# Kernel optimization log

Measured on AMD Instinct MI355X. Metric: run time of the kernel, lower is better.

## Reference

```python
import jax, jax.numpy as jnp
import numpy as np
import math

NUM_HEADS = 8
HEAD_DIM = 32  # num_units 256 / 8 heads
TIME_DIM = 8
NEG_BIG = -2.0 ** 32 + 1.0


def _ffn(x, W1, b1, W2, b2):
    # two-layer relu MLP: 1 -> time_dim -> time_dim
    h = jax.nn.relu(x @ W1 + b1)
    return jax.nn.relu(h @ W2 + b2)


def _time_gsm_kernel(t, pW1, pb1, pW2, pb2, sW1, sb1, sW2, sb2, bW1, bb1, bW2, bb2):
    # t: [B, L] timestamps -> kernel [B, L, L]
    tt = t[..., None]  # [B, L, 1]
    period = _ffn(tt, pW1, pb1, pW2, pb2)        # [B, L, td]
    qpq = (2.0 * math.pi) * period * tt           # [B, L, td]
    period_diff = qpq[:, :, None, :] - qpq[:, None, :, :]  # [B, Lq, Lk, td]
    cos_enc = jnp.cos(period_diff)
    sigma = _ffn(tt, sW1, sb1, sW2, sb2)          # [B, L, td]
    sq = sigma[:, :, None, :] + 1e-6              # [B, Lq, 1, td] bcast
    sk = sigma[:, None, :, :] + 1e-6              # [B, 1, Lk, td] bcast
    denom = sq ** 2 + sk ** 2
    t_diff = t[:, :, None] - t[:, None, :]        # [B, Lq, Lk]
    exp_enc = jnp.exp(-(t_diff[..., None] ** 2) / denom)
    local_enc = jnp.sqrt(2.0 * sq * sk / denom)
    basis = _ffn(tt, bW1, bb1, bW2, bb2)          # [B, L, td]
    basis_qk = basis[:, :, None, :] * basis[:, None, :, :]
    return jnp.sum(basis_qk * local_enc * exp_enc * cos_enc, axis=-1)  # [B, L, L]


def setup_inputs() -> dict:
    key = jax.random.key(0)
    ks = jax.random.split(key, 20)
    B, L, U = 4, 1024, 256
    td = TIME_DIM
    inp = {
        'query_input': jax.random.normal(ks[0], (B, L, U), dtype=jnp.float32),
        'input_tensor': jax.random.normal(ks[1], (B, L, U), dtype=jnp.float32),
        'input_mask': jnp.ones((B, L), dtype=jnp.int32),
        'time_inputs': jax.random.uniform(ks[2], (B, L), dtype=jnp.float32) * 100.0,
        'att_bias': jnp.zeros((1,), dtype=jnp.int32),
        'Wq': jax.random.normal(ks[3], (U, U), dtype=jnp.float32) * 0.05,
        'Wk': jax.random.normal(ks[4], (U, U), dtype=jnp.float32) * 0.05,
        'Wv': jax.random.normal(ks[5], (U, U), dtype=jnp.float32) * 0.05,
    }
    names = ['p', 's', 'b']
    i = 6
    for n in names:
        inp[n + 'W1'] = jax.random.normal(ks[i], (1, td), dtype=jnp.float32) * 0.5; i += 1
        inp[n + 'b1'] = jnp.zeros((td,), dtype=jnp.float32)
        inp[n + 'W2'] = jax.random.normal(ks[i], (td, td), dtype=jnp.float32) * 0.5; i += 1
        inp[n + 'b2'] = jnp.zeros((td,), dtype=jnp.float32)
    return inp


def reference(query_input, input_tensor, input_mask, time_inputs, att_bias,
              Wq, Wk, Wv,
              pW1, pb1, pW2, pb2, sW1, sb1, sW2, sb2, bW1, bb1, bW2, bb2):
    B, Lq, U = query_input.shape
    Lk = input_tensor.shape[1]
    H, dh = NUM_HEADS, HEAD_DIM

    Q = (query_input @ Wq).reshape(B, Lq, H, dh).transpose(0, 2, 1, 3)  # [B,H,Lq,dh]
    K = (input_tensor @ Wk).reshape(B, Lk, H, dh).transpose(0, 2, 1, 3)
    V = (input_tensor @ Wv).reshape(B, Lk, H, dh).transpose(0, 2, 1, 3)

    scale = 1.0 / math.sqrt(dh)
    scores = jnp.einsum('bhqd,bhkd->bhqk', Q, K) * scale  # [B,H,Lq,Lk]

    tk = _time_gsm_kernel(time_inputs, pW1, pb1, pW2, pb2,
                          sW1, sb1, sW2, sb2, bW1, bb1, bW2, bb2)  # [B,Lq,Lk]
    scores = scores + tk[:, None, :, :] * scale

    # key padding mask: zero-norm keys get -inf-like score
    key_masks = jnp.sign(jnp.sum(jnp.abs(K), axis=-1))  # [B,H,Lk]
    scores = jnp.where(key_masks[:, :, None, :] == 0.0, NEG_BIG, scores)

    # direction == 'forward': allow strictly row > col (strict causal)
    idx = jnp.arange(Lk)
    causal = (idx[:, None] > idx[None, :]).astype(scores.dtype)  # [Lq,Lk]
    scores = scores + (1.0 - causal) * -10000.0

    attn = jax.nn.softmax(scores, axis=-1)

    query_masks = jnp.sign(jnp.sum(jnp.abs(Q), axis=-1))  # [B,H,Lq]
    attn = attn * query_masks[..., None]
    # dropout rate 0.0 -> identity

    out = jnp.einsum('bhqk,bhkd->bhqd', attn, V)
    out = out.transpose(0, 2, 1, 3).reshape(B, Lq, U)
    out = out * input_mask.astype(jnp.float32)[..., None]
    return out
```

## Files before the change

### kernel.cpp

```cpp
#include <hip/hip_runtime.h>
#include <math.h>

#define B_DIM 4
#define L_DIM 1024
#define H_DIM 8
#define D_DIM 32
#define TD 8
#define NTILES_TOT 1056
#define SCALE 0.17677669529663687f
#define TWO_PI_F 6.2831853071795864769f

typedef unsigned short ushort_t;
typedef __attribute__((ext_vector_type(8))) short short8v;
typedef __attribute__((ext_vector_type(4))) float f32x4;

__device__ __forceinline__ int ntiles_of(int qt) { return (qt >> 1) + 1; }
__device__ __forceinline__ int off_of(int qt) {
  int m = qt >> 1;
  return (qt & 1) ? (m + 1) * (m + 1) : m * m + m;
}

__device__ __forceinline__ ushort_t f2bf(float f) {
  unsigned u = __builtin_bit_cast(unsigned, f);
  u += 0x7FFFu + ((u >> 16) & 1u);
  return (ushort_t)(u >> 16);
}
__device__ __forceinline__ float bf2f(ushort_t h) {
  return __builtin_bit_cast(float, ((unsigned)h) << 16);
}
__device__ __forceinline__ short8v pack84(float4 a, float4 b) {
  short8v r;
  r[0] = (short)f2bf(a.x); r[1] = (short)f2bf(a.y);
  r[2] = (short)f2bf(a.z); r[3] = (short)f2bf(a.w);
  r[4] = (short)f2bf(b.x); r[5] = (short)f2bf(b.y);
  r[6] = (short)f2bf(b.z); r[7] = (short)f2bf(b.w);
  return r;
}

__global__ __launch_bounds__(256) void prep_kernel(
    const float* __restrict__ t_in,
    const float* __restrict__ pW1, const float* __restrict__ pb1,
    const float* __restrict__ pW2, const float* __restrict__ pb2,
    const float* __restrict__ sW1, const float* __restrict__ sb1,
    const float* __restrict__ sW2, const float* __restrict__ sb2,
    const float* __restrict__ bW1, const float* __restrict__ bb1,
    const float* __restrict__ bW2, const float* __restrict__ bb2,
    float* __restrict__ ptf, float* __restrict__ sg, float* __restrict__ bs,
    const float* __restrict__ Xq, const float* __restrict__ Xi,
    ushort_t* __restrict__ Xfq, ushort_t* __restrict__ Xfi,
    const float* __restrict__ Wq, const float* __restrict__ Wk,
    const float* __restrict__ Wv, ushort_t* __restrict__ Wf) {
  const int blk = blockIdx.x;
  const int tid = threadIdx.x;
  if (blk < 512) {
    const int lin = blk * 256 + tid;
    const int i = lin >> 5;
    const int slot = lin & 31;
    const int z = slot >> 3, e = slot & 7;
    if (z == 3) return;
    const float* W1 = (z == 0) ? pW1 : (z == 1) ? sW1 : bW1;
    const float* b1 = (z == 0) ? pb1 : (z == 1) ? sb1 : bb1;
    const float* W2 = (z == 0) ? pW2 : (z == 1) ? sW2 : bW2;
    const float* b2 = (z == 0) ? pb2 : (z == 1) ? sb2 : bb2;
    const double t = (double)t_in[i];
    double acc = (double)b2[e];
#pragma unroll
    for (int d = 0; d < 8; ++d) {
      double hv = t * (double)W1[d] + (double)b1[d];
      hv = hv > 0.0 ? hv : 0.0;
      acc += hv * (double)W2[d * 8 + e];
    }
    acc = acc > 0.0 ? acc : 0.0;
    const size_t o = (size_t)i * TD + e;
    if (z == 0) {
      double pt = acc * t;
      ptf[o] = (float)(pt - floor(pt));
    } else if (z == 1) {
      sg[o] = (float)(acc + 1e-6);
    } else {
      bs[o] = (float)acc;
    }
  } else if (blk < 1536) {
    const int xb = blk - 512;
    const float* X = (xb < 512) ? Xq : Xi;
    ushort_t* O = (xb < 512) ? Xfq : Xfi;
    const int lin = (xb & 511) * 256 + tid;
    const int row = lin >> 5, q = lin & 31;
    const float* src = &X[(size_t)row * 256 + q * 8];
    short8v f = pack84(*(const float4*)src, *(const float4*)(src + 4));
    size_t idx = ((size_t)((row >> 4) * 8 + (q >> 2)) * 64 + (q & 3) * 16 + (row & 15)) * 8;
    *(short8v*)&O[idx] = f;
  } else {
    const int wb = blk - 1536;
    const int z = wb >> 5;
    const float* W = (z == 0) ? Wq : (z == 1) ? Wk : Wv;
    const int lin = (wb & 31) * 256 + tid;
    const int kt = lin >> 10, g = (lin >> 8) & 3, n = lin & 255;
    short8v f;
#pragma unroll
    for (int i2 = 0; i2 < 8; ++i2)
      f[i2] = (short)f2bf(W[(size_t)(kt * 32 + g * 8 + i2) * 256 + n]);
    size_t idx = ((size_t)((z * 8 + kt) * 16 + (n >> 4)) * 64 + g * 16 + (n & 15)) * 8;
    *(short8v*)&Wf[idx] = f;
  }
}

__global__ __launch_bounds__(256) void work_kernel(
    const ushort_t* __restrict__ Xfq, const ushort_t* __restrict__ Xfi,
    const ushort_t* __restrict__ Wf,
    ushort_t* __restrict__ Qf, ushort_t* __restrict__ Kf,
    ushort_t* __restrict__ Vf,
    const float* __restrict__ ptf, const float* __restrict__ sg,
    const float* __restrict__ bs, const float* __restrict__ t_in,
    float* __restrict__ tkbuf) {
  __shared__ float ptq[16][TD], ptk[32][9];
  __shared__ float qs[16][TD], qb[16][TD];
  __shared__ float ks[32][9], kb[32][9];
  __shared__ float trow[16], tcol[32];
  const int blk = blockIdx.x;
  const int tid = threadIdx.x;

  if (blk < 384) {
    const int z = blk >> 7;
    const int rem = blk & 127;
    const int m0t = (rem & 31) * 8;
    const int n0 = (rem >> 5) * 64;
    const ushort_t* Xf = (z == 0) ? Xfq : Xfi;
    const int w = tid >> 6, l = tid & 63, lg = l >> 4, lc = l & 15;
    const int wm = w >> 1, wn = w & 1;

    f32x4 acc[4][2];
#pragma unroll
    for (int mi = 0; mi < 4; ++mi)
#pragma unroll
      for (int ni = 0; ni < 2; ++ni) acc[mi][ni] = (f32x4){0.f, 0.f, 0.f, 0.f};

    for (int kt0 = 0; kt0 < 8; ++kt0) {
      short8v a[4], bfr[2];
#pragma unroll
      for (int mi = 0; mi < 4; ++mi)
        a[mi] = *(const short8v*)&Xf[((size_t)(m0t + wm * 4 + mi) * 8 + kt0) * 512 + l * 8];
#pragma unroll
      for (int ni = 0; ni < 2; ++ni)
        bfr[ni] = *(const short8v*)&Wf[((size_t)(z * 8 + kt0) * 16 + (n0 >> 4) + wn * 2 + ni) * 512 + l * 8];
#pragma unroll
      for (int mi = 0; mi < 4; ++mi)
#pragma unroll
        for (int ni = 0; ni < 2; ++ni)
          acc[mi][ni] = __builtin_amdgcn_mfma_f32_16x16x32_bf16(a[mi], bfr[ni], acc[mi][ni], 0, 0, 0);
    }

#pragma unroll
    for (int mi = 0; mi < 4; ++mi) {
#pragma unroll
      for (int ni = 0; ni < 2; ++ni) {
        const int col = n0 + wn * 32 + ni * 16 + lc;
        const int hh = col >> 5, d = col & 31;
#pragma unroll
        for (int r = 0; r < 4; ++r) {
          const int row = (m0t + wm * 4 + mi) * 16 + lg * 4 + r;
          const int bb = row >> 10, lr = row & (L_DIM - 1);
          const ushort_t bv = f2bf(acc[mi][ni][r]);
          if (z == 2) {
            Vf[(((size_t)(bb * H_DIM + hh) * 32 + (lr >> 5)) * 2 + (d >> 4)) * 512 +
               (((lr >> 3) & 3) * 16 + (d & 15)) * 8 + (lr & 7)] = bv;
          } else {
            ushort_t* of16 = (z == 0) ? Qf : Kf;
            of16[((size_t)((bb * H_DIM + hh) * 64 + (lr >> 4))) * 512 +
                 ((d >> 3) * 16 + (lr & 15)) * 8 + (d & 7)] = bv;
          }
        }
      }
    }
  } else {
    const int lin = blk - 384;
    const int b = lin / NTILES_TOT;
    const int t1 = lin - b * NTILES_TOT;
    int m = (int)sqrtf((float)t1 + 1.0f);
    while (m * m + m > t1) --m;
    while ((m + 1) * (m + 1) + (m + 1) <= t1) ++m;
    const int rem = t1 - (m * m + m);
    int qt, kt;
    if (rem <= m) { qt = 2 * m; kt = rem; }
    else          { qt = 2 * m + 1; kt = rem - (m + 1); }

    const int q0 = qt << 4, k0 = kt << 5;
    if (tid < 16 * TD) {
      int i = tid >> 3, d = tid & 7;
      size_t base = (size_t)(b * L_DIM + q0 + i) * TD + d;
      ptq[i][d] = ptf[base]; qs[i][d] = sg[base]; qb[i][d] = bs[base];
    }
    {
      int j = tid >> 3, d = tid & 7;
      size_t base = (size_t)(b * L_DIM + k0 + j) * TD + d;
      ptk[j][d] = ptf[base]; ks[j][d] = sg[base]; kb[j][d] = bs[base];
    }
    if (tid < 16) trow[tid] = t_in[b * L_DIM + q0 + tid];
    if (tid < 32) tcol[tid] = t_in[b * L_DIM + k0 + tid];
    __syncthreads();
    float* dst = &tkbuf[(size_t)(b * NTILES_TOT + off_of(qt) + kt) * 512];
#pragma unroll
    for (int pp = 0; pp < 2; ++pp) {
      int idx = tid + (pp << 8);
      int lr2 = (idx >> 2) & 63;
      int r = idx & 3;
      int i = ((lr2 >> 4) << 2) | r;
      int j = ((idx >> 8) << 4) | (lr2 & 15);
      float td2 = trow[i] - tcol[j];
      td2 *= td2;
      float a = 0.f;
#pragma unroll
      for (int d = 0; d < TD; ++d) {
        float sqd = qs[i][d], skd = ks[j][d];
        float denom = sqd * sqd + skd * skd;
        float inv = __builtin_amdgcn_rcpf(denom);
        float ee = __expf(-td2 * inv);
        float le = __builtin_amdgcn_sqrtf(2.f * sqd * skd * inv);
        float dq = ptq[i][d] - ptk[j][d];
        float ce = __cosf(TWO_PI_F * dq);
        a += qb[i][d] * kb[j][d] * (le * ee * ce);
      }
      dst[idx] = a;
    }
  }
}

__global__ __launch_bounds__(256) void attn_row0_kernel(
    const ushort_t* __restrict__ Qf, const ushort_t* __restrict__ Kf,
    const ushort_t* __restrict__ Vf, const float* __restrict__ tkbuf,
    const int* __restrict__ imask, float* __restrict__ out) {
  __shared__ __align__(16) ushort_t lds_p[4][1024];
  __shared__ float p_s[L_DIM];
  __shared__ float qsh[D_DIM];
  __shared__ float red[8][33];
  __shared__ float rtmp[4];

  const int h = blockIdx.y;
  const int b = blockIdx.z;
  const int tid = threadIdx.x;
  const int fb = (b * H_DIM + h) * 64;
  const int vb = (b * H_DIM + h) * 32;

  if (blockIdx.x == 16) {
    if (tid < D_DIM)
      qsh[tid] = bf2f(Qf[(size_t)fb * 512 + (tid >> 3) * 128 + (tid & 7)]);
    __syncthreads();

    float lmax = -1e30f;
    for (int j = tid; j < L_DIM; j += 256) {
      int i = j & 15;
      float tkv = tkbuf[(size_t)(b * NTILES_TOT + off_of(j >> 4)) * 512 +
                        (((i >> 2) << 6) | (i & 3))];
      const ushort_t* kp = &Kf[(size_t)(fb + (j >> 4)) * 512 + (j & 15) * 8];
      float dot = 0.f;
#pragma unroll
      for (int o = 0; o < 4; ++o) {
        short8v kv = *(const short8v*)&kp[o * 128];
#pragma unroll
        for (int u = 0; u < 8; ++u) dot += qsh[o * 8 + u] * bf2f((ushort_t)kv[u]);
      }
      float sc = (dot + tkv) * SCALE;
      p_s[j] = sc;
      lmax = fmaxf(lmax, sc);
    }
#pragma unroll
    for (int o = 1; o < 64; o <<= 1) lmax = fmaxf(lmax, __shfl_xor(lmax, o));
    if ((tid & 63) == 0) rtmp[tid >> 6] = lmax;
    __syncthreads();
    const float bmax = fmaxf(fmaxf(rtmp[0], rtmp[1]), fmaxf(rtmp[2], rtmp[3]));
    __syncthreads();

    float lsumv = 0.f;
    for (int j = tid; j < L_DIM; j += 256) {
      float pv = __expf(p_s[j] - bmax);
      p_s[j] = pv;
      lsumv += pv;
    }
#pragma unroll
    for (int o = 1; o < 64; o <<= 1) lsumv += __shfl_xor(lsumv, o);
    if ((tid & 63) == 0) rtmp[tid >> 6] = lsumv;
    __syncthreads();
    const float bsum = rtmp[0] + rtmp[1] + rtmp[2] + rtmp[3];

    const int g = tid >> 5, d = tid & 31;
    float a = 0.f;
    for (int j = g * 128; j < g * 128 + 128; ++j) {
      float v = bf2f(Vf[(((size_t)(vb + (j >> 5))) * 2 + (d >> 4)) * 512 +
                        (((j >> 3) & 3) * 16 + (d & 15)) * 8 + (j & 7)]);
      a = fmaf(p_s[j], v, a);
    }
    red[g][d] = a;
    __syncthreads();
    if (tid < D_DIM) {
      float acc = 0.f;
#pragma unroll
      for (int gg = 0; gg < 8; ++gg) acc += red[gg][tid];
      float qabs = 0.f;
#pragma unroll
      for (int dd = 0; dd < D_DIM; ++dd) qabs += fabsf(qsh[dd]);
      const float qmv = qabs > 0.f ? 1.f : 0.f;
      out[((size_t)b * L_DIM) * 256 + h * D_DIM + tid] =
          acc * (1.0f / bsum) * qmv * (float)imask[b * L_DIM];
    }
    return;
  }

  const int qc = (b >= 2) ? (int)blockIdx.x : 15 - (int)blockIdx.x;
  const int w = tid >> 6;
  const int l = tid & 63;
  const int lg = l >> 4;
  const int lc = l & 15;
  const int qbase = qc * 64 + w * 16;
  const int qt = qbase >> 4;

  short8v qfrag = *(const short8v*)&Qf[((size_t)(fb + qt)) * 512 + l * 8];
  float qabs_l = 0.f;
#pragma unroll
  for (int j = 0; j < 8; ++j) qabs_l += fabsf(bf2f((ushort_t)qfrag[j]));
  qabs_l += __shfl_xor(qabs_l, 16);
  qabs_l += __shfl_xor(qabs_l, 32);
  const float qm = (qabs_l > 0.f) ? 1.f : 0.f;

  f32x4 O0 = {0.f, 0.f, 0.f, 0.f};
  f32x4 O1 = {0.f, 0.f, 0.f, 0.f};
  float mrow[4] = {-1e30f, -1e30f, -1e30f, -1e30f};
  float lrow[4] = {0.f, 0.f, 0.f, 0.f};
  const float* tk_qt = &tkbuf[(size_t)(b * NTILES_TOT + off_of(qt)) * 512];
  ushort_t* Pw = lds_p[w];

  for (int kc = 0; kc <= qc; ++kc) {
    float s[4][4];
    const bool diag = (kc == qc);
#pragma unroll
    for (int kt = 0; kt < 4; ++kt) {
      short8v kfrag = *(const short8v*)&Kf[((size_t)(fb + kc * 4 + kt)) * 512 + l * 8];
      f32x4 z4 = {0.f, 0.f, 0.f, 0.f};
      f32x4 sv = __builtin_amdgcn_mfma_f32_16x16x32_bf16(qfrag, kfrag, z4, 0, 0, 0);
      float4 tk4 = *(const float4*)&tk_qt[(size_t)(kc * 2 + (kt >> 1)) * 512 + (kt & 1) * 256 + l * 4];
      float tka[4] = {tk4.x, tk4.y, tk4.z, tk4.w};
      const int col = kc * 64 + kt * 16 + lc;
#pragma unroll
      for (int r = 0; r < 4; ++r) {
        float val = (sv[r] + tka[r]) * SCALE;
        if (diag && col >= qbase + lg * 4 + r) val = -10000.0f;
        s[kt][r] = val;
      }
    }

#pragma unroll
    for (int r = 0; r < 4; ++r) {
      float tmax = fmaxf(fmaxf(s[0][r], s[1][r]), fmaxf(s[2][r], s[3][r]));
      tmax = fmaxf(tmax, __shfl_xor(tmax, 1));
      tmax = fmaxf(tmax, __shfl_xor(tmax, 2));
      tmax = fmaxf(tmax, __shfl_xor(tmax, 4));
      tmax = fmaxf(tmax, __shfl_xor(tmax, 8));
      float mnew = fmaxf(mrow[r], tmax);
      float cf = __expf(mrow[r] - mnew);
      mrow[r] = mnew;
      float p0 = __expf(s[0][r] - mnew);
      float p1 = __expf(s[1][r] - mnew);
      float p2 = __expf(s[2][r] - mnew);
      float p3 = __expf(s[3][r] - mnew);
      float psum = (p0 + p1) + (p2 + p3);
      psum += __shfl_xor(psum, 1);
      psum += __shfl_xor(psum, 2);
      psum += __shfl_xor(psum, 4);
      psum += __shfl_xor(psum, 8);
      lrow[r] = lrow[r] * cf + psum;
      O0[r] *= cf;
      O1[r] *= cf;
      const int pb = ((lc >> 3) << 7) + ((lg * 4 + r) << 3) + (lc & 7);
      Pw[pb] = f2bf(p0);
      Pw[pb + 256] = f2bf(p1);
      Pw[pb + 512] = f2bf(p2);
      Pw[pb + 768] = f2bf(p3);
    }

#pragma unroll
    for (int kh = 0; kh < 2; ++kh) {
      short8v pfrag = *(const short8v*)&Pw[(kh * 64 + l) * 8];
      const size_t vbase = ((size_t)(vb + kc * 2 + kh)) * 1024 + l * 8;
      short8v vf0 = *(const short8v*)&Vf[vbase];
      short8v vf1 = *(const short8v*)&Vf[vbase + 512];
      O0 = __builtin_amdgcn_mfma_f32_16x16x32_bf16(pfrag, vf0, O0, 0, 0, 0);
      O1 = __builtin_amdgcn_mfma_f32_16x16x32_bf16(pfrag, vf1, O1, 0, 0, 0);
    }
  }

#pragma unroll
  for (int r = 0; r < 4; ++r) {
    const int rr = lg * 4 + r;
    const int qrow = qbase + rr;
    float qmr = __shfl(qm, rr);
    float im = (float)imask[b * L_DIM + qrow];
    float scl = (1.f / lrow[r]) * qmr * im;
    if (qrow != 0) {
      float* op = &out[((size_t)(b * L_DIM + qrow)) * 256 + h * D_DIM];
      op[lc] = O0[r] * scl;
      op[16 + lc] = O1[r] * scl;
    }
  }
}

extern "C" void kernel_launch(void* const* d_in, const int* in_sizes, int n_in,
                              void* d_out, int out_size, void* d_ws, size_t ws_size,
                              hipStream_t stream) {
  (void)in_sizes; (void)n_in; (void)out_size; (void)ws_size;
  const float* query = (const float*)d_in[0];
  const float* input = (const float*)d_in[1];
  const int* imask = (const int*)d_in[2];
  const float* t_in = (const float*)d_in[3];
  const float* Wq = (const float*)d_in[5];
  const float* Wk = (const float*)d_in[6];
  const float* Wv = (const float*)d_in[7];
  const float* pW1 = (const float*)d_in[8],  *pb1 = (const float*)d_in[9];
  const float* pW2 = (const float*)d_in[10], *pb2 = (const float*)d_in[11];
  const float* sW1 = (const float*)d_in[12], *sb1 = (const float*)d_in[13];
  const float* sW2 = (const float*)d_in[14], *sb2 = (const float*)d_in[15];
  const float* bW1 = (const float*)d_in[16], *bb1 = (const float*)d_in[17];
  const float* bW2 = (const float*)d_in[18], *bb2 = (const float*)d_in[19];
  float* out = (float*)d_out;

  const int M = B_DIM * L_DIM;
  char* p = (char*)d_ws;
  ushort_t* Qf = (ushort_t*)p;  p += (size_t)M * 256 * 2;
  ushort_t* Kf = (ushort_t*)p;  p += (size_t)M * 256 * 2;
  ushort_t* Vf = (ushort_t*)p;  p += (size_t)M * 256 * 2;
  ushort_t* Xfq = (ushort_t*)p; p += (size_t)M * 256 * 2;
  ushort_t* Xfi = (ushort_t*)p; p += (size_t)M * 256 * 2;
  ushort_t* Wfb = (ushort_t*)p; p += (size_t)3 * 256 * 256 * 2;
  float* ptf = (float*)p;       p += (size_t)M * TD * 4;
  float* sg = (float*)p;        p += (size_t)M * TD * 4;
  float* bs = (float*)p;        p += (size_t)M * TD * 4;
  float* tkbuf = (float*)p;

  prep_kernel<<<1632, 256, 0, stream>>>(
      t_in, pW1, pb1, pW2, pb2, sW1, sb1, sW2, sb2, bW1, bb1, bW2, bb2,
      ptf, sg, bs, query, input, Xfq, Xfi, Wq, Wk, Wv, Wfb);
  work_kernel<<<384 + B_DIM * NTILES_TOT, 256, 0, stream>>>(
      Xfq, Xfi, Wfb, Qf, Kf, Vf, ptf, sg, bs, t_in, tkbuf);
  attn_row0_kernel<<<dim3(17, H_DIM, B_DIM), 256, 0, stream>>>(
      Qf, Kf, Vf, tkbuf, imask, out);
}
```

Measured before the change: 62.08 us.

## Fuse bf16 conversion into QKV GEMM, split time kernel, restructure attention loop

```diff
diff --git a/kernel.cpp b/kernel.cpp
--- a/kernel.cpp
+++ b/kernel.cpp
@@ -8,7 +8,6 @@
 #define TD 8
 #define NTILES_TOT 1056
 #define SCALE 0.17677669529663687f
-#define TWO_PI_F 6.2831853071795864769f
 
 typedef unsigned short ushort_t;
 typedef __attribute__((ext_vector_type(8))) short short8v;
@@ -37,23 +36,87 @@
   return r;
 }
 
-__global__ __launch_bounds__(256) void prep_kernel(
-    const float* __restrict__ t_in,
+__global__ __launch_bounds__(256) void prep_gemm_kernel(
+    const float* __restrict__ Xq, const float* __restrict__ Xi,
+    const float* __restrict__ Wq, const float* __restrict__ Wk,
+    const float* __restrict__ Wv, const float* __restrict__ t_in,
     const float* __restrict__ pW1, const float* __restrict__ pb1,
     const float* __restrict__ pW2, const float* __restrict__ pb2,
     const float* __restrict__ sW1, const float* __restrict__ sb1,
     const float* __restrict__ sW2, const float* __restrict__ sb2,
     const float* __restrict__ bW1, const float* __restrict__ bb1,
     const float* __restrict__ bW2, const float* __restrict__ bb2,
-    float* __restrict__ ptf, float* __restrict__ sg, float* __restrict__ bs,
-    const float* __restrict__ Xq, const float* __restrict__ Xi,
-    ushort_t* __restrict__ Xfq, ushort_t* __restrict__ Xfi,
-    const float* __restrict__ Wq, const float* __restrict__ Wk,
-    const float* __restrict__ Wv, ushort_t* __restrict__ Wf) {
+    ushort_t* __restrict__ Qf, ushort_t* __restrict__ Kf,
+    ushort_t* __restrict__ Vf,
+    float* __restrict__ ptf, float* __restrict__ sg, float* __restrict__ bs) {
   const int blk = blockIdx.x;
   const int tid = threadIdx.x;
-  if (blk < 512) {
-    const int lin = blk * 256 + tid;
+
+  if (blk < 384) {
+    const int z = blk >> 7;
+    const int rem = blk & 127;
+    const int m0 = (rem & 31) * 128;
+    const int n0 = (rem >> 5) * 64;
+    const float* X = (z == 0) ? Xq : Xi;
+    const float* W = (z == 0) ? Wq : (z == 1) ? Wk : Wv;
+    const int w = tid >> 6, l = tid & 63, lg = l >> 4, lc = l & 15;
+    const int wm = w >> 1, wn = w & 1;
+
+    f32x4 acc[4][2];
+#pragma unroll
+    for (int mi = 0; mi < 4; ++mi)
+#pragma unroll
+      for (int ni = 0; ni < 2; ++ni) acc[mi][ni] = (f32x4){0.f, 0.f, 0.f, 0.f};
+
+    for (int kt0 = 0; kt0 < 8; ++kt0) {
+      short8v a[4], bfr[2];
+#pragma unroll
+      for (int mi = 0; mi < 4; ++mi) {
+        const float* xp = &X[(size_t)(m0 + (wm * 4 + mi) * 16 + lc) * 256 + kt0 * 32 + lg * 8];
+        a[mi] = pack84(*(const float4*)xp, *(const float4*)(xp + 4));
+      }
+#pragma unroll
+      for (int ni = 0; ni < 2; ++ni) {
+        const int ncol = n0 + (wn * 2 + ni) * 16 + lc;
+        short8v bf;
+#pragma unroll
+        for (int j = 0; j < 8; ++j)
+          bf[j] = (short)f2bf(W[(size_t)(kt0 * 32 + lg * 8 + j) * 256 + ncol]);
+        bfr[ni] = bf;
+      }
+#pragma unroll
+      for (int mi = 0; mi < 4; ++mi)
+#pragma unroll
+        for (int ni = 0; ni < 2; ++ni)
+          acc[mi][ni] = __builtin_amdgcn_mfma_f32_16x16x32_bf16(a[mi], bfr[ni], acc[mi][ni], 0, 0, 0);
+    }
+
+#pragma unroll
+    for (int mi = 0; mi < 4; ++mi) {
+#pragma unroll
+      for (int ni = 0; ni < 2; ++ni) {
+        const int col = n0 + wn * 32 + ni * 16 + lc;
+        const int hh = col >> 5, d = col & 31;
+#pragma unroll
+        for (int r = 0; r < 4; ++r) {
+          const int row = m0 + (wm * 4 + mi) * 16 + lg * 4 + r;
+          const int bb = row >> 10, lr = row & (L_DIM - 1);
+          float v = acc[mi][ni][r];
+          if (z == 0) v *= SCALE;
+          const ushort_t bv = f2bf(v);
+          if (z == 2) {
+            Vf[(((size_t)(bb * H_DIM + hh) * 32 + (lr >> 5)) * 2 + (d >> 4)) * 512 +
+               (((lr >> 3) & 3) * 16 + (d & 15)) * 8 + (lr & 7)] = bv;
+          } else {
+            ushort_t* of16 = (z == 0) ? Qf : Kf;
+            of16[((size_t)((bb * H_DIM + hh) * 64 + (lr >> 4))) * 512 +
+                 ((d >> 3) * 16 + (lr & 15)) * 8 + (d & 7)] = bv;
+          }
+        }
+      }
+    }
+  } else {
+    const int lin = (blk - 384) * 256 + tid;
     const int i = lin >> 5;
     const int slot = lin & 31;
     const int z = slot >> 3, e = slot & 7;
@@ -80,152 +143,90 @@
     } else {
       bs[o] = (float)acc;
     }
-  } else if (blk < 1536) {
-    const int xb = blk - 512;
-    const float* X = (xb < 512) ? Xq : Xi;
-    ushort_t* O = (xb < 512) ? Xfq : Xfi;
-    const int lin = (xb & 511) * 256 + tid;
-    const int row = lin >> 5, q = lin & 31;
-    const float* src = &X[(size_t)row * 256 + q * 8];
-    short8v f = pack84(*(const float4*)src, *(const float4*)(src + 4));
-    size_t idx = ((size_t)((row >> 4) * 8 + (q >> 2)) * 64 + (q & 3) * 16 + (row & 15)) * 8;
-    *(short8v*)&O[idx] = f;
-  } else {
-    const int wb = blk - 1536;
-    const int z = wb >> 5;
-    const float* W = (z == 0) ? Wq : (z == 1) ? Wk : Wv;
-    const int lin = (wb & 31) * 256 + tid;
-    const int kt = lin >> 10, g = (lin >> 8) & 3, n = lin & 255;
-    short8v f;
-#pragma unroll
-    for (int i2 = 0; i2 < 8; ++i2)
-      f[i2] = (short)f2bf(W[(size_t)(kt * 32 + g * 8 + i2) * 256 + n]);
-    size_t idx = ((size_t)((z * 8 + kt) * 16 + (n >> 4)) * 64 + g * 16 + (n & 15)) * 8;
-    *(short8v*)&Wf[idx] = f;
-  }
-}
-
-__global__ __launch_bounds__(256) void work_kernel(
-    const ushort_t* __restrict__ Xfq, const ushort_t* __restrict__ Xfi,
-    const ushort_t* __restrict__ Wf,
-    ushort_t* __restrict__ Qf, ushort_t* __restrict__ Kf,
-    ushort_t* __restrict__ Vf,
+  }
+}
+
+__global__ __launch_bounds__(256) void tk_kernel(
     const float* __restrict__ ptf, const float* __restrict__ sg,
     const float* __restrict__ bs, const float* __restrict__ t_in,
     float* __restrict__ tkbuf) {
-  __shared__ float ptq[16][TD], ptk[32][9];
-  __shared__ float qs[16][TD], qb[16][TD];
-  __shared__ float ks[32][9], kb[32][9];
+  __shared__ __align__(16) float ptq[16 * 8], qsh[16 * 8], qbh[16 * 8];
+  __shared__ __align__(16) float ptk[32 * 12], ksh[32 * 12], kbh[32 * 12];
   __shared__ float trow[16], tcol[32];
   const int blk = blockIdx.x;
   const int tid = threadIdx.x;
 
-  if (blk < 384) {
-    const int z = blk >> 7;
-    const int rem = blk & 127;
-    const int m0t = (rem & 31) * 8;
-    const int n0 = (rem >> 5) * 64;
-    const ushort_t* Xf = (z == 0) ? Xfq : Xfi;
-    const int w = tid >> 6, l = tid & 63, lg = l >> 4, lc = l & 15;
-    const int wm = w >> 1, wn = w & 1;
-
-    f32x4 acc[4][2];
-#pragma unroll
-    for (int mi = 0; mi < 4; ++mi)
-#pragma unroll
-      for (int ni = 0; ni < 2; ++ni) acc[mi][ni] = (f32x4){0.f, 0.f, 0.f, 0.f};
-
-    for (int kt0 = 0; kt0 < 8; ++kt0) {
-      short8v a[4], bfr[2];
-#pragma unroll
-      for (int mi = 0; mi < 4; ++mi)
-        a[mi] = *(const short8v*)&Xf[((size_t)(m0t + wm * 4 + mi) * 8 + kt0) * 512 + l * 8];
-#pragma unroll
-      for (int ni = 0; ni < 2; ++ni)
-        bfr[ni] = *(const short8v*)&Wf[((size_t)(z * 8 + kt0) * 16 + (n0 >> 4) + wn * 2 + ni) * 512 + l * 8];
-#pragma unroll
-      for (int mi = 0; mi < 4; ++mi)
-#pragma unroll
-        for (int ni = 0; ni < 2; ++ni)
-          acc[mi][ni] = __builtin_amdgcn_mfma_f32_16x16x32_bf16(a[mi], bfr[ni], acc[mi][ni], 0, 0, 0);
-    }
-
-#pragma unroll
-    for (int mi = 0; mi < 4; ++mi) {
-#pragma unroll
-      for (int ni = 0; ni < 2; ++ni) {
-        const int col = n0 + wn * 32 + ni * 16 + lc;
-        const int hh = col >> 5, d = col & 31;
-#pragma unroll
-        for (int r = 0; r < 4; ++r) {
-          const int row = (m0t + wm * 4 + mi) * 16 + lg * 4 + r;
-          const int bb = row >> 10, lr = row & (L_DIM - 1);
-          const ushort_t bv = f2bf(acc[mi][ni][r]);
-          if (z == 2) {
-            Vf[(((size_t)(bb * H_DIM + hh) * 32 + (lr >> 5)) * 2 + (d >> 4)) * 512 +
-               (((lr >> 3) & 3) * 16 + (d & 15)) * 8 + (lr & 7)] = bv;
-          } else {
-            ushort_t* of16 = (z == 0) ? Qf : Kf;
-            of16[((size_t)((bb * H_DIM + hh) * 64 + (lr >> 4))) * 512 +
-                 ((d >> 3) * 16 + (lr & 15)) * 8 + (d & 7)] = bv;
-          }
-        }
-      }
-    }
-  } else {
-    const int lin = blk - 384;
-    const int b = lin / NTILES_TOT;
-    const int t1 = lin - b * NTILES_TOT;
-    int m = (int)sqrtf((float)t1 + 1.0f);
-    while (m * m + m > t1) --m;
-    while ((m + 1) * (m + 1) + (m + 1) <= t1) ++m;
-    const int rem = t1 - (m * m + m);
-    int qt, kt;
-    if (rem <= m) { qt = 2 * m; kt = rem; }
-    else          { qt = 2 * m + 1; kt = rem - (m + 1); }
-
-    const int q0 = qt << 4, k0 = kt << 5;
-    if (tid < 16 * TD) {
-      int i = tid >> 3, d = tid & 7;
-      size_t base = (size_t)(b * L_DIM + q0 + i) * TD + d;
-      ptq[i][d] = ptf[base]; qs[i][d] = sg[base]; qb[i][d] = bs[base];
-    }
-    {
-      int j = tid >> 3, d = tid & 7;
-      size_t base = (size_t)(b * L_DIM + k0 + j) * TD + d;
-      ptk[j][d] = ptf[base]; ks[j][d] = sg[base]; kb[j][d] = bs[base];
-    }
-    if (tid < 16) trow[tid] = t_in[b * L_DIM + q0 + tid];
-    if (tid < 32) tcol[tid] = t_in[b * L_DIM + k0 + tid];
-    __syncthreads();
-    float* dst = &tkbuf[(size_t)(b * NTILES_TOT + off_of(qt) + kt) * 512];
-#pragma unroll
-    for (int pp = 0; pp < 2; ++pp) {
-      int idx = tid + (pp << 8);
-      int lr2 = (idx >> 2) & 63;
-      int r = idx & 3;
-      int i = ((lr2 >> 4) << 2) | r;
-      int j = ((idx >> 8) << 4) | (lr2 & 15);
-      float td2 = trow[i] - tcol[j];
-      td2 *= td2;
-      float a = 0.f;
-#pragma unroll
-      for (int d = 0; d < TD; ++d) {
-        float sqd = qs[i][d], skd = ks[j][d];
-        float denom = sqd * sqd + skd * skd;
-        float inv = __builtin_amdgcn_rcpf(denom);
-        float ee = __expf(-td2 * inv);
-        float le = __builtin_amdgcn_sqrtf(2.f * sqd * skd * inv);
-        float dq = ptq[i][d] - ptk[j][d];
-        float ce = __cosf(TWO_PI_F * dq);
-        a += qb[i][d] * kb[j][d] * (le * ee * ce);
-      }
-      dst[idx] = a;
-    }
-  }
-}
-
-__global__ __launch_bounds__(256) void attn_row0_kernel(
+  const int b = blk / NTILES_TOT;
+  const int t1 = blk - b * NTILES_TOT;
+  int m = (int)sqrtf((float)t1 + 1.0f);
+  while (m * m + m > t1) --m;
+  while ((m + 1) * (m + 1) + (m + 1) <= t1) ++m;
+  const int rem = t1 - (m * m + m);
+  int qt, kt;
+  if (rem <= m) { qt = 2 * m; kt = rem; }
+  else          { qt = 2 * m + 1; kt = rem - (m + 1); }
+  const int q0 = qt << 4, k0 = kt << 5;
+
+  if (tid < 16) trow[tid] = t_in[b * L_DIM + q0 + tid];
+  if (tid < 32) tcol[tid] = t_in[b * L_DIM + k0 + tid];
+  if (tid < 128) {
+    const int i = tid >> 3, d = tid & 7;
+    const size_t base = (size_t)(b * L_DIM + q0 + i) * TD + d;
+    ptq[i * 8 + d] = ptf[base];
+    qsh[i * 8 + d] = sg[base];
+    qbh[i * 8 + d] = bs[base];
+  }
+  {
+    const int j = tid >> 3, d = tid & 7;
+    const size_t base = (size_t)(b * L_DIM + k0 + j) * TD + d;
+    ptk[j * 12 + d] = ptf[base];
+    ksh[j * 12 + d] = sg[base];
+    kbh[j * 12 + d] = bs[base];
+  }
+  __syncthreads();
+
+  const int r = tid & 3;
+  const int lr2 = tid >> 2;
+  const int i = ((lr2 >> 4) << 2) | r;
+  float pq[8], qs_[8], qb_[8];
+  *(float4*)&pq[0]  = *(const float4*)&ptq[i * 8];
+  *(float4*)&pq[4]  = *(const float4*)&ptq[i * 8 + 4];
+  *(float4*)&qs_[0] = *(const float4*)&qsh[i * 8];
+  *(float4*)&qs_[4] = *(const float4*)&qsh[i * 8 + 4];
+  *(float4*)&qb_[0] = *(const float4*)&qbh[i * 8];
+  *(float4*)&qb_[4] = *(const float4*)&qbh[i * 8 + 4];
+  const float ti = trow[i];
+
+  float* dst = &tkbuf[(size_t)(b * NTILES_TOT + off_of(qt) + kt) * 512];
+#pragma unroll
+  for (int pp = 0; pp < 2; ++pp) {
+    const int j = pp * 16 + (lr2 & 15);
+    float td2 = ti - tcol[j];
+    td2 *= td2;
+    float pk[8], ks_[8], kb_[8];
+    *(float4*)&pk[0]  = *(const float4*)&ptk[j * 12];
+    *(float4*)&pk[4]  = *(const float4*)&ptk[j * 12 + 4];
+    *(float4*)&ks_[0] = *(const float4*)&ksh[j * 12];
+    *(float4*)&ks_[4] = *(const float4*)&ksh[j * 12 + 4];
+    *(float4*)&kb_[0] = *(const float4*)&kbh[j * 12];
+    *(float4*)&kb_[4] = *(const float4*)&kbh[j * 12 + 4];
+    float a = 0.f;
+#pragma unroll
+    for (int d = 0; d < TD; ++d) {
+      const float sqd = qs_[d], skd = ks_[d];
+      const float denom = sqd * sqd + skd * skd;
+      const float inv = __builtin_amdgcn_rcpf(denom);
+      const float ee = __expf(-td2 * inv);
+      const float le = __builtin_amdgcn_sqrtf(2.f * sqd * skd * inv);
+      const float dq = __builtin_fabsf(pq[d] - pk[d]);
+      const float ce = __builtin_amdgcn_cosf(dq);
+      a += qb_[d] * kb_[d] * (le * ee * ce);
+    }
+    dst[tid + (pp << 8)] = a * SCALE;
+  }
+}
+
+__global__ __launch_bounds__(256, 4) void attn_row0_kernel(
     const ushort_t* __restrict__ Qf, const ushort_t* __restrict__ Kf,
     const ushort_t* __restrict__ Vf, const float* __restrict__ tkbuf,
     const int* __restrict__ imask, float* __restrict__ out) {
@@ -259,7 +260,7 @@
 #pragma unroll
         for (int u = 0; u < 8; ++u) dot += qsh[o * 8 + u] * bf2f((ushort_t)kv[u]);
       }
-      float sc = (dot + tkv) * SCALE;
+      float sc = dot + tkv;
       p_s[j] = sc;
       lmax = fmaxf(lmax, sc);
     }
@@ -305,7 +306,7 @@
     return;
   }
 
-  const int qc = (b >= 2) ? (int)blockIdx.x : 15 - (int)blockIdx.x;
+  const int qc = 15 - (int)blockIdx.x;
   const int w = tid >> 6;
   const int l = tid & 63;
   const int lg = l >> 4;
@@ -329,21 +330,46 @@
   ushort_t* Pw = lds_p[w];
 
   for (int kc = 0; kc <= qc; ++kc) {
+    const bool diag = (kc == qc);
+    const size_t kb_ = ((size_t)(fb + kc * 4)) * 512 + l * 8;
+    short8v kf0 = *(const short8v*)&Kf[kb_];
+    short8v kf1 = *(const short8v*)&Kf[kb_ + 512];
+    short8v kf2 = *(const short8v*)&Kf[kb_ + 1024];
+    short8v kf3 = *(const short8v*)&Kf[kb_ + 1536];
+    const size_t tb_ = (size_t)(kc * 2) * 512 + l * 4;
+    float4 t0 = *(const float4*)&tk_qt[tb_];
+    float4 t1 = *(const float4*)&tk_qt[tb_ + 256];
+    float4 t2 = *(const float4*)&tk_qt[tb_ + 512];
+    float4 t3 = *(const float4*)&tk_qt[tb_ + 768];
+    const size_t vb_ = ((size_t)(vb + kc * 2)) * 1024 + l * 8;
+    short8v vf0 = *(const short8v*)&Vf[vb_];
+    short8v vf1 = *(const short8v*)&Vf[vb_ + 512];
+    short8v vf2 = *(const short8v*)&Vf[vb_ + 1024];
+    short8v vf3 = *(const short8v*)&Vf[vb_ + 1536];
+
+    f32x4 z4 = {0.f, 0.f, 0.f, 0.f};
+    __builtin_amdgcn_s_setprio(1);
+    f32x4 sv0 = __builtin_amdgcn_mfma_f32_16x16x32_bf16(qfrag, kf0, z4, 0, 0, 0);
+    f32x4 sv1 = __builtin_amdgcn_mfma_f32_16x16x32_bf16(qfrag, kf1, z4, 0, 0, 0);
+    f32x4 sv2 = __builtin_amdgcn_mfma_f32_16x16x32_bf16(qfrag, kf2, z4, 0, 0, 0);
+    f32x4 sv3 = __builtin_amdgcn_mfma_f32_16x16x32_bf16(qfrag, kf3, z4, 0, 0, 0);
+    __builtin_amdgcn_s_setprio(0);
+
     float s[4][4];
-    const bool diag = (kc == qc);
-#pragma unroll
-    for (int kt = 0; kt < 4; ++kt) {
-      short8v kfrag = *(const short8v*)&Kf[((size_t)(fb + kc * 4 + kt)) * 512 + l * 8];
-      f32x4 z4 = {0.f, 0.f, 0.f, 0.f};
-      f32x4 sv = __builtin_amdgcn_mfma_f32_16x16x32_bf16(qfrag, kfrag, z4, 0, 0, 0);
-      float4 tk4 = *(const float4*)&tk_qt[(size_t)(kc * 2 + (kt >> 1)) * 512 + (kt & 1) * 256 + l * 4];
-      float tka[4] = {tk4.x, tk4.y, tk4.z, tk4.w};
-      const int col = kc * 64 + kt * 16 + lc;
-#pragma unroll
-      for (int r = 0; r < 4; ++r) {
-        float val = (sv[r] + tka[r]) * SCALE;
-        if (diag && col >= qbase + lg * 4 + r) val = -10000.0f;
-        s[kt][r] = val;
+#pragma unroll
+    for (int r = 0; r < 4; ++r) {
+      s[0][r] = sv0[r] + (&t0.x)[r];
+      s[1][r] = sv1[r] + (&t1.x)[r];
+      s[2][r] = sv2[r] + (&t2.x)[r];
+      s[3][r] = sv3[r] + (&t3.x)[r];
+    }
+    if (diag) {
+#pragma unroll
+      for (int kt = 0; kt < 4; ++kt) {
+        const int col = kc * 64 + kt * 16 + lc;
+#pragma unroll
+        for (int r = 0; r < 4; ++r)
+          if (col >= qbase + lg * 4 + r) s[kt][r] = -10000.0f;
       }
     }
 
@@ -361,12 +387,7 @@
       float p1 = __expf(s[1][r] - mnew);
       float p2 = __expf(s[2][r] - mnew);
       float p3 = __expf(s[3][r] - mnew);
-      float psum = (p0 + p1) + (p2 + p3);
-      psum += __shfl_xor(psum, 1);
-      psum += __shfl_xor(psum, 2);
-      psum += __shfl_xor(psum, 4);
-      psum += __shfl_xor(psum, 8);
-      lrow[r] = lrow[r] * cf + psum;
+      lrow[r] = lrow[r] * cf + ((p0 + p1) + (p2 + p3));
       O0[r] *= cf;
       O1[r] *= cf;
       const int pb = ((lc >> 3) << 7) + ((lg * 4 + r) << 3) + (lc & 7);
@@ -375,20 +396,22 @@
       Pw[pb + 512] = f2bf(p2);
       Pw[pb + 768] = f2bf(p3);
     }
-
-#pragma unroll
-    for (int kh = 0; kh < 2; ++kh) {
-      short8v pfrag = *(const short8v*)&Pw[(kh * 64 + l) * 8];
-      const size_t vbase = ((size_t)(vb + kc * 2 + kh)) * 1024 + l * 8;
-      short8v vf0 = *(const short8v*)&Vf[vbase];
-      short8v vf1 = *(const short8v*)&Vf[vbase + 512];
-      O0 = __builtin_amdgcn_mfma_f32_16x16x32_bf16(pfrag, vf0, O0, 0, 0, 0);
-      O1 = __builtin_amdgcn_mfma_f32_16x16x32_bf16(pfrag, vf1, O1, 0, 0, 0);
-    }
+    short8v pf0 = *(const short8v*)&Pw[l * 8];
+    short8v pf1 = *(const short8v*)&Pw[(64 + l) * 8];
+    __builtin_amdgcn_s_setprio(1);
+    O0 = __builtin_amdgcn_mfma_f32_16x16x32_bf16(pf0, vf0, O0, 0, 0, 0);
+    O1 = __builtin_amdgcn_mfma_f32_16x16x32_bf16(pf0, vf1, O1, 0, 0, 0);
+    O0 = __builtin_amdgcn_mfma_f32_16x16x32_bf16(pf1, vf2, O0, 0, 0, 0);
+    O1 = __builtin_amdgcn_mfma_f32_16x16x32_bf16(pf1, vf3, O1, 0, 0, 0);
+    __builtin_amdgcn_s_setprio(0);
   }
 
 #pragma unroll
   for (int r = 0; r < 4; ++r) {
+    lrow[r] += __shfl_xor(lrow[r], 1);
+    lrow[r] += __shfl_xor(lrow[r], 2);
+    lrow[r] += __shfl_xor(lrow[r], 4);
+    lrow[r] += __shfl_xor(lrow[r], 8);
     const int rr = lg * 4 + r;
     const int qrow = qbase + rr;
     float qmr = __shfl(qm, rr);
@@ -426,19 +449,16 @@
   ushort_t* Qf = (ushort_t*)p;  p += (size_t)M * 256 * 2;
   ushort_t* Kf = (ushort_t*)p;  p += (size_t)M * 256 * 2;
   ushort_t* Vf = (ushort_t*)p;  p += (size_t)M * 256 * 2;
-  ushort_t* Xfq = (ushort_t*)p; p += (size_t)M * 256 * 2;
-  ushort_t* Xfi = (ushort_t*)p; p += (size_t)M * 256 * 2;
-  ushort_t* Wfb = (ushort_t*)p; p += (size_t)3 * 256 * 256 * 2;
   float* ptf = (float*)p;       p += (size_t)M * TD * 4;
   float* sg = (float*)p;        p += (size_t)M * TD * 4;
   float* bs = (float*)p;        p += (size_t)M * TD * 4;
   float* tkbuf = (float*)p;
 
-  prep_kernel<<<1632, 256, 0, stream>>>(
-      t_in, pW1, pb1, pW2, pb2, sW1, sb1, sW2, sb2, bW1, bb1, bW2, bb2,
-      ptf, sg, bs, query, input, Xfq, Xfi, Wq, Wk, Wv, Wfb);
-  work_kernel<<<384 + B_DIM * NTILES_TOT, 256, 0, stream>>>(
-      Xfq, Xfi, Wfb, Qf, Kf, Vf, ptf, sg, bs, t_in, tkbuf);
+  prep_gemm_kernel<<<384 + 512, 256, 0, stream>>>(
+      query, input, Wq, Wk, Wv, t_in,
+      pW1, pb1, pW2, pb2, sW1, sb1, sW2, sb2, bW1, bb1, bW2, bb2,
+      Qf, Kf, Vf, ptf, sg, bs);
+  tk_kernel<<<B_DIM * NTILES_TOT, 256, 0, stream>>>(ptf, sg, bs, t_in, tkbuf);
   attn_row0_kernel<<<dim3(17, H_DIM, B_DIM), 256, 0, stream>>>(
       Qf, Kf, Vf, tkbuf, imask, out);
 }
```

Result: slower. 74.71 us (+20.3%).
